# Kernel optimization log

Hardware: AMD Instinct MI355X
Metric: run time of the kernel (lower is better)

The kernel has to match this reference:

```python
import jax, jax.numpy as jnp
import numpy as np

BATCH, IN, HID, OUT = 8192, 784, 4096, 10


def setup_inputs() -> dict:
    key = jax.random.key(0)
    k_x, k_w1, k_b1, k_w2, k_b2 = jax.random.split(key, 5)
    return {
        "x": jax.random.normal(k_x, (BATCH, IN), dtype=jnp.float32),
        "W1": jax.random.normal(k_w1, (HID, IN), dtype=jnp.float32) * 0.05,
        "b1": jax.random.normal(k_b1, (HID,), dtype=jnp.float32) * 0.05,
        "W2": jax.random.normal(k_w2, (OUT, HID), dtype=jnp.float32) * 0.05,
        "b2": jax.random.normal(k_b2, (OUT,), dtype=jnp.float32) * 0.05,
    }


def reference(x, W1, b1, W2, b2):
    # x: [B, 784] -- first layer, so the input is NOT binarized (BNN convention
    # for in_features == 784); only the weight is sign-quantized.
    x = x.reshape(-1, IN)
    Wb1 = jnp.sign(W1)                       # binarized weights in {-1, 0, +1}
    h = jnp.einsum("bi,hi->bh", x, Wb1) + b1  # BinarizeLinear fc1
    h = jnp.clip(h, -1.0, 1.0)               # Hardtanh
    out = jnp.einsum("bh,oh->bo", h, W2) + b2  # plain float fc2
    return out
```

## Files before the change

### kernel.cpp

```cpp
#include <hip/hip_runtime.h>
#include <cstdint>


#define BATCH 8192
#define IN_F  784
#define HID   4096
#define OUT_F 10
#define KP    832
#define NKT   13
#define BM    256
#define BN    256
#define BK    64
#define NCT   (HID / BN)
#define HCS   264

typedef unsigned short u16;
typedef __attribute__((ext_vector_type(4))) unsigned short u16x4;
typedef __attribute__((ext_vector_type(8)))  _Float16 f16x8;
typedef __attribute__((ext_vector_type(4)))  float    f32x4;
typedef __attribute__((ext_vector_type(16))) float    f32x16;

#define BARRIER() do { asm volatile("" ::: "memory"); \
                       __builtin_amdgcn_s_barrier();  \
                       asm volatile("" ::: "memory"); } while (0)
#define WAITV(n)  asm volatile("s_waitcnt vmcnt(" #n ")" ::: "memory")

__device__ __forceinline__ u16 f2h(float f) {
  union { _Float16 h; u16 u; } c;
  c.h = (_Float16)f;
  return c.u;
}

__device__ __forceinline__ void gl_lds16(const void* g, void* l) {
  __builtin_amdgcn_global_load_lds(
      (const __attribute__((address_space(1))) uint32_t*)g,
      (__attribute__((address_space(3))) uint32_t*)l, 16, 0, 0);
}

__global__ void prep_kernel(const float* __restrict__ x, const float* __restrict__ W1,
                            const float* __restrict__ W2,
                            u16* __restrict__ xh, u16* __restrict__ wh,
                            u16* __restrict__ w2h) {
  const int stride = gridDim.x * blockDim.x;
  const int gid = blockIdx.x * blockDim.x + threadIdx.x;
  const int KP4 = KP / 4;
  const int IN4 = IN_F / 4;
  const float4* x4 = (const float4*)x;
  const float4* w4 = (const float4*)W1;
  for (int i = gid; i < BATCH * KP4; i += stride) {
    int b = i / KP4, k = i - b * KP4;
    u16x4 o = {0, 0, 0, 0};
    if (k < IN4) {
      float4 v = x4[(size_t)b * IN4 + k];
      o[0] = f2h(v.x); o[1] = f2h(v.y); o[2] = f2h(v.z); o[3] = f2h(v.w);
    }
    *(u16x4*)&xh[(size_t)b * KP + k * 4] = o;
  }
  for (int i = gid; i < HID * KP4; i += stride) {
    int h = i / KP4, k = i - h * KP4;
    u16x4 o = {0, 0, 0, 0};
    if (k < IN4) {
      float4 v = w4[(size_t)h * IN4 + k];
      o[0] = v.x > 0.f ? 0x3C00 : (v.x < 0.f ? 0xBC00 : 0);
      o[1] = v.y > 0.f ? 0x3C00 : (v.y < 0.f ? 0xBC00 : 0);
      o[2] = v.z > 0.f ? 0x3C00 : (v.z < 0.f ? 0xBC00 : 0);
      o[3] = v.w > 0.f ? 0x3C00 : (v.w < 0.f ? 0xBC00 : 0);
    }
    *(u16x4*)&wh[(size_t)h * KP + k * 4] = o;
  }
  for (int i = gid; i < 16 * HID; i += stride) {
    int o = i >> 12, k = i & (HID - 1);
    w2h[i] = (o < OUT_F) ? f2h(W2[o * HID + k]) : (u16)0;
  }
}

__global__ void __launch_bounds__(512, 2) gemm_kernel(
    const u16* __restrict__ xh, const u16* __restrict__ wh,
    const u16* __restrict__ w2h, const float* __restrict__ b1,
    float* __restrict__ part) {
  __shared__ union {
    struct { u16 A[2][BM * BK]; u16 B[2][BN * BK]; } m;
    struct { u16 hc[128 * HCS]; u16 w2[16 * 256]; } e;
  } sm;

  const int t   = threadIdx.x;
  const int ct  = blockIdx.x;
  const int br  = blockIdx.y;
  const int w   = t >> 6;
  const int l   = t & 63;
  const int wm  = w >> 2;
  const int wn  = w & 3;
  const int lo  = l & 31;
  const int hi  = l >> 5;
  const int g   = l >> 4;
  const int r16 = l & 15;

  const int  srow  = t >> 3;
  const int  sslot = (t & 7) ^ (srow & 7);
  const u16* gA = xh + (size_t)(br * BM) * KP + sslot * 8;
  const u16* gB = wh + (size_t)(ct * BN) * KP + sslot * 8;

  auto stage = [&](int tile) {
    const int b = tile & 1;
#pragma unroll
    for (int c = 0; c < 4; ++c)
      gl_lds16(gA + (size_t)(c * 64 + srow) * KP + tile * BK,
               &sm.m.A[b][c * 4096 + t * 8]);
#pragma unroll
    for (int c = 0; c < 4; ++c)
      gl_lds16(gB + (size_t)(c * 64 + srow) * KP + tile * BK,
               &sm.m.B[b][c * 4096 + t * 8]);
  };
  auto rdA = [&](int p, int mi, int s) -> f16x8 {
    int row = mi * 64 + wm * 32 + lo;
    return *(const f16x8*)&sm.m.A[p][row * 64 + (((s * 2 + hi) ^ (row & 7)) << 3)];
  };
  auto rdB = [&](int p, int nh, int s) -> f16x8 {
    int row = nh * 128 + wn * 32 + lo;
    return *(const f16x8*)&sm.m.B[p][row * 64 + (((s * 2 + hi) ^ (row & 7)) << 3)];
  };

  f32x16 acc[4][2] = {};

  stage(0);

  for (int tt = 0; tt < NKT; ++tt) {
    const int p = tt & 1;
#pragma unroll
    for (int s = 0; s < 4; ++s) {
      if (s == 0) {
        if (tt + 1 < NKT) { stage(tt + 1); WAITV(8); }
        else              { WAITV(0); }
        BARRIER();
      }
      f16x8 af[4], bf[2];
#pragma unroll
      for (int nh = 0; nh < 2; ++nh) bf[nh] = rdB(p, nh, s);
#pragma unroll
      for (int mi = 0; mi < 4; ++mi) af[mi] = rdA(p, mi, s);
      if (s == 3) {
        asm volatile("s_waitcnt lgkmcnt(0)" ::: "memory");
        __builtin_amdgcn_sched_barrier(0);
        BARRIER();
      }
      __builtin_amdgcn_s_setprio(1);
#pragma unroll
      for (int mi = 0; mi < 4; ++mi)
#pragma unroll
        for (int nh = 0; nh < 2; ++nh)
          acc[mi][nh] = __builtin_amdgcn_mfma_f32_32x32x16_f16(af[mi], bf[nh], acc[mi][nh], 0, 0, 0);
      __builtin_amdgcn_s_setprio(0);
    }
  }

  {
    int row = t >> 5, sp = t & 31;
    int ls = (sp & 24) | ((sp ^ row) & 7);
    gl_lds16(w2h + (size_t)row * HID + ct * BN + ls * 8, &sm.e.w2[t * 8]);
  }
  float b1v[2];
#pragma unroll
  for (int nh = 0; nh < 2; ++nh) b1v[nh] = b1[ct * BN + nh * 128 + wn * 32 + lo];

  float* partBase = part + ((size_t)ct * BATCH + br * BM) * 16;

#pragma unroll
  for (int p = 0; p < 2; ++p) {
    if (p == 1) BARRIER();
#pragma unroll
    for (int mi = 0; mi < 2; ++mi)
#pragma unroll
      for (int nh = 0; nh < 2; ++nh)
#pragma unroll
        for (int r = 0; r < 16; ++r) {
          float v = acc[p * 2 + mi][nh][r] + b1v[nh];
          v = fminf(fmaxf(v, -1.f), 1.f);
          int crow = (r & 3) + 8 * (r >> 2) + 4 * hi;
          sm.e.hc[(mi * 64 + wm * 32 + crow) * HCS + nh * 128 + wn * 32 + lo] = f2h(v);
        }
    if (p == 0) { WAITV(0); }
    BARRIER();
    f32x4 acc2 = {};
#pragma unroll
    for (int kk = 0; kk < 8; ++kk) {
      f16x8 a2 = *(const f16x8*)&sm.e.hc[(w * 16 + r16) * HCS + kk * 32 + g * 8];
      int s   = kk * 4 + g;
      int sp2 = (s & 24) | ((s ^ r16) & 7);
      f16x8 b2f = *(const f16x8*)&sm.e.w2[r16 * 256 + sp2 * 8];
      acc2 = __builtin_amdgcn_mfma_f32_16x16x32_f16(a2, b2f, acc2, 0, 0, 0);
    }
#pragma unroll
    for (int r = 0; r < 4; ++r)
      partBase[(size_t)(p * 128 + w * 16 + g * 4 + r) * 16 + r16] = acc2[r];
  }
}

__global__ void reduce_kernel(const float* __restrict__ part, const float* __restrict__ b2,
                              float* __restrict__ out) {
  int i = blockIdx.x * blockDim.x + threadIdx.x;
  if (i >= BATCH * OUT_F) return;
  int b = i / OUT_F, o = i - b * OUT_F;
  float acc = b2[o];
#pragma unroll
  for (int c = 0; c < NCT; ++c)
    acc += part[((size_t)c * BATCH + b) * 16 + o];
  out[i] = acc;
}

extern "C" void kernel_launch(void* const* d_in, const int* in_sizes, int n_in,
                              void* d_out, int out_size, void* d_ws, size_t ws_size,
                              hipStream_t stream) {
  const float* x  = (const float*)d_in[0];
  const float* W1 = (const float*)d_in[1];
  const float* b1 = (const float*)d_in[2];
  const float* W2 = (const float*)d_in[3];
  const float* b2 = (const float*)d_in[4];
  float* out = (float*)d_out;

  u16* xh  = (u16*)d_ws;
  u16* wh  = xh + (size_t)BATCH * KP;
  u16* w2h = wh + (size_t)HID * KP;
  float* part = (float*)(w2h + 16 * HID);

  hipLaunchKernelGGL(prep_kernel, dim3(2048), dim3(256), 0, stream, x, W1, W2, xh, wh, w2h);
  hipLaunchKernelGGL(gemm_kernel, dim3(NCT, BATCH / BM), dim3(512), 0, stream,
                     xh, wh, w2h, b1, part);
  hipLaunchKernelGGL(reduce_kernel, dim3((BATCH * OUT_F + 255) / 256), dim3(256), 0, stream,
                     part, b2, out);
}
```

Before: 72.24 us.

## Double-buffer MFMA fragments in registers and cut per-tile barriers to one

Restructures the main GEMM loop so LDS fragment reads for the next k-slice are issued while the MFMAs for the current slice execute, using two register sets for the A/B fragments. The next tile's first fragments are read right after a single per-tile barrier, replacing the previous pattern of two barriers per tile. This is meant to hide LDS latency behind matrix-core work and reduce synchronisation stalls. The extra fragment registers add pressure on an already tight register budget under launch_bounds(512,2), which risks spills or lower occupancy.

```diff
diff --git a/kernel.cpp b/kernel.cpp
--- a/kernel.cpp
+++ b/kernel.cpp
@@ -24,6 +24,7 @@
                        __builtin_amdgcn_s_barrier();  \
                        asm volatile("" ::: "memory"); } while (0)
 #define WAITV(n)  asm volatile("s_waitcnt vmcnt(" #n ")" ::: "memory")
+#define WAITL0()  asm volatile("s_waitcnt lgkmcnt(0)" ::: "memory")
 
 __device__ __forceinline__ u16 f2h(float f) {
   union { _Float16 h; u16 u; } c;
@@ -111,48 +112,54 @@
       gl_lds16(gB + (size_t)(c * 64 + srow) * KP + tile * BK,
                &sm.m.B[b][c * 4096 + t * 8]);
   };
-  auto rdA = [&](int p, int mi, int s) -> f16x8 {
+  auto rdA = [&](int p, int mi, int kk) -> f16x8 {
     int row = mi * 64 + wm * 32 + lo;
-    return *(const f16x8*)&sm.m.A[p][row * 64 + (((s * 2 + hi) ^ (row & 7)) << 3)];
+    return *(const f16x8*)&sm.m.A[p][row * 64 + (((kk * 2 + hi) ^ (row & 7)) << 3)];
   };
-  auto rdB = [&](int p, int nh, int s) -> f16x8 {
+  auto rdB = [&](int p, int nh, int kk) -> f16x8 {
     int row = nh * 128 + wn * 32 + lo;
-    return *(const f16x8*)&sm.m.B[p][row * 64 + (((s * 2 + hi) ^ (row & 7)) << 3)];
+    return *(const f16x8*)&sm.m.B[p][row * 64 + (((kk * 2 + hi) ^ (row & 7)) << 3)];
   };
 
   f32x16 acc[4][2] = {};
+  f16x8 af[2][4], bf[2][2];
+
+#define RD(S, P, KK) do {                                             \
+    _Pragma("unroll") for (int mi_ = 0; mi_ < 4; ++mi_) af[S][mi_] = rdA(P, mi_, KK); \
+    _Pragma("unroll") for (int nh_ = 0; nh_ < 2; ++nh_) bf[S][nh_] = rdB(P, nh_, KK); \
+  } while (0)
+#define MFMA8(S) do {                                                 \
+    __builtin_amdgcn_s_setprio(1);                                    \
+    _Pragma("unroll") for (int mi_ = 0; mi_ < 4; ++mi_)               \
+      _Pragma("unroll") for (int nh_ = 0; nh_ < 2; ++nh_)             \
+        acc[mi_][nh_] = __builtin_amdgcn_mfma_f32_32x32x16_f16(       \
+            af[S][mi_], bf[S][nh_], acc[mi_][nh_], 0, 0, 0);          \
+    __builtin_amdgcn_s_setprio(0);                                    \
+  } while (0)
 
   stage(0);
+  WAITV(0);
+  BARRIER();
+  RD(0, 0, 0);
 
   for (int tt = 0; tt < NKT; ++tt) {
-    const int p = tt & 1;
-#pragma unroll
-    for (int s = 0; s < 4; ++s) {
-      if (s == 0) {
-        if (tt + 1 < NKT) { stage(tt + 1); WAITV(8); }
-        else              { WAITV(0); }
-        BARRIER();
-      }
-      f16x8 af[4], bf[2];
-#pragma unroll
-      for (int nh = 0; nh < 2; ++nh) bf[nh] = rdB(p, nh, s);
-#pragma unroll
-      for (int mi = 0; mi < 4; ++mi) af[mi] = rdA(p, mi, s);
-      if (s == 3) {
-        asm volatile("s_waitcnt lgkmcnt(0)" ::: "memory");
-        __builtin_amdgcn_sched_barrier(0);
-        BARRIER();
-      }
-      __builtin_amdgcn_s_setprio(1);
-#pragma unroll
-      for (int mi = 0; mi < 4; ++mi)
-#pragma unroll
-        for (int nh = 0; nh < 2; ++nh)
-          acc[mi][nh] = __builtin_amdgcn_mfma_f32_32x32x16_f16(af[mi], bf[nh], acc[mi][nh], 0, 0, 0);
-      __builtin_amdgcn_s_setprio(0);
-    }
-  }
-
+    const int  p    = tt & 1;
+    const bool more = (tt + 1 < NKT);
+    if (more) stage(tt + 1);
+    RD(1, p, 1);  MFMA8(0);
+    RD(0, p, 2);  MFMA8(1);
+    RD(1, p, 3);  MFMA8(0);
+    if (more) {
+      WAITL0();
+      WAITV(0);
+      BARRIER();
+      RD(0, p ^ 1, 0);
+    }
+    MFMA8(1);
+  }
+
+  WAITL0();
+  BARRIER();
   {
     int row = t >> 5, sp = t & 31;
     int ls = (sp & 24) | ((sp ^ row) & 7);
```

Result: faster. 67.26 us (-6.9%).

## Triple-buffer B tiles and spread global-to-LDS loads across k sub-steps

Applied to the files above, without the earlier changes.

Adds a third LDS buffer for the weight (B) tiles so B is prefetched two k-tiles ahead. The A prefetch is split into halves issued at different k sub-steps, with barriers around every MFMA sub-step. Launch bounds drop from two blocks per CU to one, since the larger LDS footprint no longer fits two blocks. The aim is to hide global load latency better, at the cost of occupancy and extra barriers per k-tile.

```diff
diff --git a/kernel.cpp b/kernel.cpp
--- a/kernel.cpp
+++ b/kernel.cpp
@@ -24,6 +24,7 @@
                        __builtin_amdgcn_s_barrier();  \
                        asm volatile("" ::: "memory"); } while (0)
 #define WAITV(n)  asm volatile("s_waitcnt vmcnt(" #n ")" ::: "memory")
+#define WAITL0()  asm volatile("s_waitcnt lgkmcnt(0)" ::: "memory")
 
 __device__ __forceinline__ u16 f2h(float f) {
   union { _Float16 h; u16 u; } c;
@@ -74,12 +75,12 @@
   }
 }
 
-__global__ void __launch_bounds__(512, 2) gemm_kernel(
+__global__ void __launch_bounds__(512, 1) gemm_kernel(
     const u16* __restrict__ xh, const u16* __restrict__ wh,
     const u16* __restrict__ w2h, const float* __restrict__ b1,
     float* __restrict__ part) {
   __shared__ union {
-    struct { u16 A[2][BM * BK]; u16 B[2][BN * BK]; } m;
+    struct { u16 A[2][BM * BK]; u16 B[3][BN * BK]; } m;
     struct { u16 hc[128 * HCS]; u16 w2[16 * 256]; } e;
   } sm;
 
@@ -100,57 +101,67 @@
   const u16* gA = xh + (size_t)(br * BM) * KP + sslot * 8;
   const u16* gB = wh + (size_t)(ct * BN) * KP + sslot * 8;
 
-  auto stage = [&](int tile) {
+  auto stA2 = [&](int tile, int h) {
     const int b = tile & 1;
 #pragma unroll
-    for (int c = 0; c < 4; ++c)
+    for (int c = 2 * h; c < 2 * h + 2; ++c)
       gl_lds16(gA + (size_t)(c * 64 + srow) * KP + tile * BK,
                &sm.m.A[b][c * 4096 + t * 8]);
+  };
+  auto stB = [&](int tile, int s) {
 #pragma unroll
     for (int c = 0; c < 4; ++c)
       gl_lds16(gB + (size_t)(c * 64 + srow) * KP + tile * BK,
-               &sm.m.B[b][c * 4096 + t * 8]);
-  };
-  auto rdA = [&](int p, int mi, int s) -> f16x8 {
+               &sm.m.B[s][c * 4096 + t * 8]);
+  };
+  auto rdA = [&](int p, int mi, int kk) -> f16x8 {
     int row = mi * 64 + wm * 32 + lo;
-    return *(const f16x8*)&sm.m.A[p][row * 64 + (((s * 2 + hi) ^ (row & 7)) << 3)];
-  };
-  auto rdB = [&](int p, int nh, int s) -> f16x8 {
+    return *(const f16x8*)&sm.m.A[p][row * 64 + (((kk * 2 + hi) ^ (row & 7)) << 3)];
+  };
+  auto rdB = [&](int s, int nh, int kk) -> f16x8 {
     int row = nh * 128 + wn * 32 + lo;
-    return *(const f16x8*)&sm.m.B[p][row * 64 + (((s * 2 + hi) ^ (row & 7)) << 3)];
+    return *(const f16x8*)&sm.m.B[s][row * 64 + (((kk * 2 + hi) ^ (row & 7)) << 3)];
   };
 
   f32x16 acc[4][2] = {};
 
-  stage(0);
-
+  stA2(0, 0); stA2(0, 1);
+  stB(0, 0);
+  stB(1, 1);
+  WAITV(4);
+  BARRIER();
+
+  int bs = 0;
   for (int tt = 0; tt < NKT; ++tt) {
-    const int p = tt & 1;
-#pragma unroll
-    for (int s = 0; s < 4; ++s) {
-      if (s == 0) {
-        if (tt + 1 < NKT) { stage(tt + 1); WAITV(8); }
-        else              { WAITV(0); }
-        BARRIER();
-      }
+    const int  p      = tt & 1;
+    const int  bs2    = (bs >= 1) ? bs - 1 : 2;
+    const bool a_more = (tt + 1 < NKT);
+    const bool b_more = (tt + 2 < NKT);
+#pragma unroll
+    for (int kk = 0; kk < 4; ++kk) {
       f16x8 af[4], bf[2];
 #pragma unroll
-      for (int nh = 0; nh < 2; ++nh) bf[nh] = rdB(p, nh, s);
-#pragma unroll
-      for (int mi = 0; mi < 4; ++mi) af[mi] = rdA(p, mi, s);
-      if (s == 3) {
-        asm volatile("s_waitcnt lgkmcnt(0)" ::: "memory");
-        __builtin_amdgcn_sched_barrier(0);
-        BARRIER();
-      }
+      for (int mi = 0; mi < 4; ++mi) af[mi] = rdA(p, mi, kk);
+#pragma unroll
+      for (int nh = 0; nh < 2; ++nh) bf[nh] = rdB(bs, nh, kk);
+      if      (kk == 0) { if (a_more) stA2(tt + 1, 0); }
+      else if (kk == 1) { if (a_more) stA2(tt + 1, 1); }
+      else if (kk == 2) { if (b_more) stB(tt + 2, bs2); }
+      else              { if (tt < NKT - 2) WAITV(4); else WAITV(0); }
+      BARRIER();
+      WAITL0();
+      __builtin_amdgcn_sched_barrier(0);
       __builtin_amdgcn_s_setprio(1);
 #pragma unroll
       for (int mi = 0; mi < 4; ++mi)
 #pragma unroll
         for (int nh = 0; nh < 2; ++nh)
-          acc[mi][nh] = __builtin_amdgcn_mfma_f32_32x32x16_f16(af[mi], bf[nh], acc[mi][nh], 0, 0, 0);
+          acc[mi][nh] = __builtin_amdgcn_mfma_f32_32x32x16_f16(
+              af[mi], bf[nh], acc[mi][nh], 0, 0, 0);
       __builtin_amdgcn_s_setprio(0);
-    }
+      BARRIER();
+    }
+    bs = (bs == 2) ? 0 : bs + 1;
   }
 
   {
```

Measured after the change: 71.41 us. About the same (-1.2%).
